# Optimization experiments

Measured on AMD Instinct MI355X. Metric: run time of the kernel, lower is better.

Reference implementation:

```python
import jax, jax.numpy as jnp
from jax import lax
import numpy as np

B, M, N, NUM_ITER = 8192, 256, 512, 16


def setup_inputs() -> dict:
    key = jax.random.key(0)
    k1, k2, k3, k4, k5 = jax.random.split(key, 5)
    y = jax.random.normal(k1, (B, M), dtype=jnp.float32)
    # Scale S/D/W so the unrolled recurrence stays numerically stable over 16 steps
    S = jax.random.normal(k2, (N, N), dtype=jnp.float32) * (0.9 / np.sqrt(N))
    W = jax.random.normal(k3, (N, M), dtype=jnp.float32) * (0.1 / np.sqrt(M))
    D = jax.random.normal(k4, (N, N), dtype=jnp.float32) * (1.0 / np.sqrt(N))
    thr = jax.random.uniform(k5, (1, 1), dtype=jnp.float32) * 0.1
    return {"y": y, "S": S, "W": W, "D": D, "thr": thr, "numIter": NUM_ITER}


def soft_thr(u, theta):
    return jax.nn.relu(u - theta) - jax.nn.relu(-u - theta)


def reference(y, S, W, D, thr, numIter):
    # Batch-first rewrite of: d = (D.T @ soft_thr(D @ (S@d.T + W@y.T), thr)).T
    Wy = y @ W.T  # (B, N), invariant across iterations
    d0 = jnp.zeros((y.shape[0], S.shape[0]), dtype=y.dtype)

    def step(d, _):
        z = d @ S.T + Wy          # (B, N)
        u = z @ D.T               # (B, N)  == (D @ z.T).T
        d_new = soft_thr(u, thr) @ D  # (B, N) == (D.T @ s.T).T
        return d_new, d_new

    _, ds = lax.scan(step, d0, None, length=numIter)
    # Original returns list [d0, d1, ..., d_numIter]; stack as one array
    return jnp.concatenate([d0[None], ds], axis=0)  # (numIter+1, B, N)
```

## Files before the change

### kernel.cpp

```cpp
#include <hip/hip_runtime.h>

#define B_SZ 8192
#define M_SZ 256
#define N_SZ 512
#define TB 64
#define THREADS 1024
#define LDP 520
#define LDPY 264
#define NITER 16

typedef _Float16 half8 __attribute__((ext_vector_type(8)));
typedef _Float16 half4 __attribute__((ext_vector_type(4)));
typedef float floatx4 __attribute__((ext_vector_type(4)));

__global__ void conv_kernel(const float* __restrict__ W, const float* __restrict__ D,
                            _Float16* __restrict__ Wf, _Float16* __restrict__ Df,
                            _Float16* __restrict__ Dtf) {
  int i = blockIdx.x * blockDim.x + threadIdx.x;
  if (i < N_SZ * N_SZ) {
    float d = D[i];
    Df[i] = (_Float16)d;
    int r = i >> 9;
    int c = i & (N_SZ - 1);
    Dtf[c * N_SZ + r] = (_Float16)d;
  }
  if (i < N_SZ * M_SZ) Wf[i] = (_Float16)W[i];
}

__global__ __launch_bounds__(256) void ecomp_kernel(const float* __restrict__ S,
                                                    const float* __restrict__ D,
                                                    _Float16* __restrict__ Ef) {
  __shared__ float Dst[8 * N_SZ];
  const int tid = threadIdx.x;
  const int r0 = blockIdx.x * 8;
  for (int i = tid; i < 8 * N_SZ; i += 256) Dst[i] = D[(size_t)r0 * N_SZ + i];
  __syncthreads();
  float acc[8][2];
#pragma unroll
  for (int r = 0; r < 8; ++r) acc[r][0] = acc[r][1] = 0.f;
#pragma unroll 4
  for (int j = 0; j < N_SZ; ++j) {
    float s0 = S[(size_t)j * N_SZ + tid];
    float s1 = S[(size_t)j * N_SZ + tid + 256];
#pragma unroll
    for (int r = 0; r < 8; ++r) {
      float dv = Dst[r * N_SZ + j];
      acc[r][0] += dv * s0;
      acc[r][1] += dv * s1;
    }
  }
#pragma unroll
  for (int r = 0; r < 8; ++r) {
    Ef[(size_t)(r0 + r) * N_SZ + tid] = (_Float16)acc[r][0];
    Ef[(size_t)(r0 + r) * N_SZ + tid + 256] = (_Float16)acc[r][1];
  }
}

__global__ __launch_bounds__(THREADS) void ista_kernel(
    const float* __restrict__ y, const _Float16* __restrict__ Ef,
    const _Float16* __restrict__ Df, const _Float16* __restrict__ Dtf,
    const _Float16* __restrict__ Wf, const float* __restrict__ thrp,
    float* __restrict__ out) {
  __shared__ _Float16 bufA[TB * LDP];
  __shared__ _Float16 bufB[TB * LDP];

  const int tid = threadIdx.x;
  const int wave = tid >> 6;
  const int lane = tid & 63;
  const int m16 = lane & 15;
  const int q = lane >> 4;
  const int rowBase = blockIdx.x * TB;
  const int colBase = wave * 32;

  {
    const int r = tid >> 4;
    const int c0 = (tid & 15) << 4;
    const float* src = y + (size_t)(rowBase + r) * M_SZ + c0;
#pragma unroll
    for (int j = 0; j < 16; j += 4) {
      float4 v = *reinterpret_cast<const float4*>(src + j);
      _Float16* dst = &bufA[r * LDPY + c0 + j];
      dst[0] = (_Float16)v.x;
      dst[1] = (_Float16)v.y;
      dst[2] = (_Float16)v.z;
      dst[3] = (_Float16)v.w;
    }
  }
  __syncthreads();

  floatx4 acc[4][2];

#pragma unroll
  for (int rt = 0; rt < 4; ++rt) acc[rt][0] = acc[rt][1] = (floatx4){0.f, 0.f, 0.f, 0.f};
#pragma unroll 2
  for (int ks = 0; ks < M_SZ / 32; ++ks) {
    half8 a0 = *reinterpret_cast<const half8*>(&bufA[m16 * LDPY + ks * 32 + q * 8]);
    half8 a1 = *reinterpret_cast<const half8*>(&bufA[(16 + m16) * LDPY + ks * 32 + q * 8]);
    half8 a2 = *reinterpret_cast<const half8*>(&bufA[(32 + m16) * LDPY + ks * 32 + q * 8]);
    half8 a3 = *reinterpret_cast<const half8*>(&bufA[(48 + m16) * LDPY + ks * 32 + q * 8]);
#pragma unroll
    for (int ct = 0; ct < 2; ++ct) {
      half8 b = *reinterpret_cast<const half8*>(Wf + (size_t)(colBase + ct * 16 + m16) * M_SZ + ks * 32 + q * 8);
      acc[0][ct] = __builtin_amdgcn_mfma_f32_16x16x32_f16(a0, b, acc[0][ct], 0, 0, 0);
      acc[1][ct] = __builtin_amdgcn_mfma_f32_16x16x32_f16(a1, b, acc[1][ct], 0, 0, 0);
      acc[2][ct] = __builtin_amdgcn_mfma_f32_16x16x32_f16(a2, b, acc[2][ct], 0, 0, 0);
      acc[3][ct] = __builtin_amdgcn_mfma_f32_16x16x32_f16(a3, b, acc[3][ct], 0, 0, 0);
    }
  }
#pragma unroll
  for (int rt = 0; rt < 4; ++rt)
#pragma unroll
    for (int ct = 0; ct < 2; ++ct)
#pragma unroll
      for (int r = 0; r < 4; ++r)
        bufB[(rt * 16 + q * 4 + r) * LDP + colBase + ct * 16 + m16] = (_Float16)acc[rt][ct][r];
  __syncthreads();

  auto gemmK512 = [&](const _Float16* Abuf, const _Float16* __restrict__ Bmat) {
    const _Float16* arow = Abuf + m16 * LDP + q * 8;
    const _Float16* brow0 = Bmat + (size_t)(colBase + m16) * N_SZ + q * 8;
    const _Float16* brow1 = Bmat + (size_t)(colBase + 16 + m16) * N_SZ + q * 8;
#pragma unroll 2
    for (int ks = 0; ks < N_SZ / 32; ++ks) {
      half8 a0 = *reinterpret_cast<const half8*>(arow + ks * 32);
      half8 a1 = *reinterpret_cast<const half8*>(arow + 16 * LDP + ks * 32);
      half8 a2 = *reinterpret_cast<const half8*>(arow + 32 * LDP + ks * 32);
      half8 a3 = *reinterpret_cast<const half8*>(arow + 48 * LDP + ks * 32);
      half8 b0 = *reinterpret_cast<const half8*>(brow0 + ks * 32);
      half8 b1 = *reinterpret_cast<const half8*>(brow1 + ks * 32);
      acc[0][0] = __builtin_amdgcn_mfma_f32_16x16x32_f16(a0, b0, acc[0][0], 0, 0, 0);
      acc[0][1] = __builtin_amdgcn_mfma_f32_16x16x32_f16(a0, b1, acc[0][1], 0, 0, 0);
      acc[1][0] = __builtin_amdgcn_mfma_f32_16x16x32_f16(a1, b0, acc[1][0], 0, 0, 0);
      acc[1][1] = __builtin_amdgcn_mfma_f32_16x16x32_f16(a1, b1, acc[1][1], 0, 0, 0);
      acc[2][0] = __builtin_amdgcn_mfma_f32_16x16x32_f16(a2, b0, acc[2][0], 0, 0, 0);
      acc[2][1] = __builtin_amdgcn_mfma_f32_16x16x32_f16(a2, b1, acc[2][1], 0, 0, 0);
      acc[3][0] = __builtin_amdgcn_mfma_f32_16x16x32_f16(a3, b0, acc[3][0], 0, 0, 0);
      acc[3][1] = __builtin_amdgcn_mfma_f32_16x16x32_f16(a3, b1, acc[3][1], 0, 0, 0);
    }
  };

#pragma unroll
  for (int rt = 0; rt < 4; ++rt) acc[rt][0] = acc[rt][1] = (floatx4){0.f, 0.f, 0.f, 0.f};
  gemmK512(bufB, Df);
  half4 ch[4][2];
#pragma unroll
  for (int rt = 0; rt < 4; ++rt)
#pragma unroll
    for (int ct = 0; ct < 2; ++ct)
#pragma unroll
      for (int r = 0; r < 4; ++r) ch[rt][ct][r] = (_Float16)acc[rt][ct][r];

  {
    int* za = reinterpret_cast<int*>(bufA);
    for (int i = tid; i < TB * LDP / 2; i += THREADS) za[i] = 0;
    float4 z4 = {0.f, 0.f, 0.f, 0.f};
    float4* o4 = reinterpret_cast<float4*>(out + (size_t)rowBase * N_SZ);
    for (int i = tid; i < TB * N_SZ / 4; i += THREADS) o4[i] = z4;
  }
  __syncthreads();

  const float thrv = *thrp;

#pragma unroll 1
  for (int it = 1; it <= NITER; ++it) {
#pragma unroll
    for (int rt = 0; rt < 4; ++rt) acc[rt][0] = acc[rt][1] = (floatx4){0.f, 0.f, 0.f, 0.f};
    gemmK512(bufA, Ef);
#pragma unroll
    for (int rt = 0; rt < 4; ++rt)
#pragma unroll
      for (int ct = 0; ct < 2; ++ct)
#pragma unroll
        for (int r = 0; r < 4; ++r) {
          float u = acc[rt][ct][r] + (float)ch[rt][ct][r];
          float s = fmaxf(u - thrv, 0.f) - fmaxf(-u - thrv, 0.f);
          bufB[(rt * 16 + q * 4 + r) * LDP + colBase + ct * 16 + m16] = (_Float16)s;
        }
    __syncthreads();

#pragma unroll
    for (int rt = 0; rt < 4; ++rt) acc[rt][0] = acc[rt][1] = (floatx4){0.f, 0.f, 0.f, 0.f};
    gemmK512(bufB, Dtf);
#pragma unroll
    for (int rt = 0; rt < 4; ++rt)
#pragma unroll
      for (int ct = 0; ct < 2; ++ct)
#pragma unroll
        for (int r = 0; r < 4; ++r)
          bufA[(rt * 16 + q * 4 + r) * LDP + colBase + ct * 16 + m16] = (_Float16)acc[rt][ct][r];
    __syncthreads();

    float* oslice = out + ((size_t)it * B_SZ + rowBase) * N_SZ;
#pragma unroll
    for (int i = tid; i < TB * N_SZ / 8; i += THREADS) {
      int r = i >> 6;
      int c8 = (i & 63) << 3;
      half8 h = *reinterpret_cast<const half8*>(&bufA[r * LDP + c8]);
      float4 lo = {(float)h[0], (float)h[1], (float)h[2], (float)h[3]};
      float4 hi = {(float)h[4], (float)h[5], (float)h[6], (float)h[7]};
      float* dst = oslice + (size_t)r * N_SZ + c8;
      *reinterpret_cast<float4*>(dst) = lo;
      *reinterpret_cast<float4*>(dst + 4) = hi;
    }
  }
}

extern "C" void kernel_launch(void* const* d_in, const int* in_sizes, int n_in,
                              void* d_out, int out_size, void* d_ws, size_t ws_size,
                              hipStream_t stream) {
  const float* y = (const float*)d_in[0];
  const float* S = (const float*)d_in[1];
  const float* W = (const float*)d_in[2];
  const float* D = (const float*)d_in[3];
  const float* thr = (const float*)d_in[4];
  float* out = (float*)d_out;

  char* ws = (char*)d_ws;
  _Float16* Ef = (_Float16*)(ws);
  _Float16* Df = (_Float16*)(ws + 512 * 1024);
  _Float16* Dtf = (_Float16*)(ws + 1024 * 1024);
  _Float16* Wf = (_Float16*)(ws + 1536 * 1024);

  conv_kernel<<<(N_SZ * N_SZ + 255) / 256, 256, 0, stream>>>(W, D, Wf, Df, Dtf);
  ecomp_kernel<<<N_SZ / 8, 256, 0, stream>>>(S, D, Ef);
  ista_kernel<<<B_SZ / TB, THREADS, 0, stream>>>(y, Ef, Df, Dtf, Wf, thr, out);
}
```

Measured before the change: 848.2 us.

## Halve batch tile, swizzle LDS, reorder iteration and stream output directly

The ISTA kernel batch tile drops from 64 to 32 rows, so twice as many blocks run and each wave holds half the accumulators. The padded LDS rows become an XOR-swizzled layout, and the loop is reordered so each iteration's D^T GEMM result goes straight from registers to global memory with nontemporal stores, which removes the separate LDS-to-global copy pass. The first soft-threshold now starts from the c term, the last E GEMM is skipped, and ecomp_kernel is rewritten with smaller blocks and no shared memory. Each block reloads the weight matrices from global/L2 for fewer rows, and the scattered scalar nontemporal stores may coalesce less well than the old float4 writes.

```diff
diff --git a/kernel.cpp b/kernel.cpp
--- a/kernel.cpp
+++ b/kernel.cpp
@@ -3,14 +3,11 @@
 #define B_SZ 8192
 #define M_SZ 256
 #define N_SZ 512
-#define TB 64
+#define TB 32
 #define THREADS 1024
-#define LDP 520
-#define LDPY 264
 #define NITER 16
 
 typedef _Float16 half8 __attribute__((ext_vector_type(8)));
-typedef _Float16 half4 __attribute__((ext_vector_type(4)));
 typedef float floatx4 __attribute__((ext_vector_type(4)));
 
 __global__ void conv_kernel(const float* __restrict__ W, const float* __restrict__ D,
@@ -27,182 +24,188 @@
   if (i < N_SZ * M_SZ) Wf[i] = (_Float16)W[i];
 }
 
-__global__ __launch_bounds__(256) void ecomp_kernel(const float* __restrict__ S,
+__global__ __launch_bounds__(512) void ecomp_kernel(const float* __restrict__ S,
                                                     const float* __restrict__ D,
                                                     _Float16* __restrict__ Ef) {
-  __shared__ float Dst[8 * N_SZ];
   const int tid = threadIdx.x;
-  const int r0 = blockIdx.x * 8;
-  for (int i = tid; i < 8 * N_SZ; i += 256) Dst[i] = D[(size_t)r0 * N_SZ + i];
-  __syncthreads();
-  float acc[8][2];
-#pragma unroll
-  for (int r = 0; r < 8; ++r) acc[r][0] = acc[r][1] = 0.f;
-#pragma unroll 4
+  const int r0 = blockIdx.x * 2;
+  float a0 = 0.f, a1 = 0.f;
+#pragma unroll 8
   for (int j = 0; j < N_SZ; ++j) {
-    float s0 = S[(size_t)j * N_SZ + tid];
-    float s1 = S[(size_t)j * N_SZ + tid + 256];
-#pragma unroll
-    for (int r = 0; r < 8; ++r) {
-      float dv = Dst[r * N_SZ + j];
-      acc[r][0] += dv * s0;
-      acc[r][1] += dv * s1;
-    }
-  }
-#pragma unroll
-  for (int r = 0; r < 8; ++r) {
-    Ef[(size_t)(r0 + r) * N_SZ + tid] = (_Float16)acc[r][0];
-    Ef[(size_t)(r0 + r) * N_SZ + tid + 256] = (_Float16)acc[r][1];
-  }
-}
-
-__global__ __launch_bounds__(THREADS) void ista_kernel(
+    float s = S[(size_t)j * N_SZ + tid];
+    a0 += D[(size_t)r0 * N_SZ + j] * s;
+    a1 += D[(size_t)(r0 + 1) * N_SZ + j] * s;
+  }
+  Ef[(size_t)r0 * N_SZ + tid] = (_Float16)a0;
+  Ef[(size_t)(r0 + 1) * N_SZ + tid] = (_Float16)a1;
+}
+
+__global__ __launch_bounds__(THREADS, 4) void ista_kernel(
     const float* __restrict__ y, const _Float16* __restrict__ Ef,
     const _Float16* __restrict__ Df, const _Float16* __restrict__ Dtf,
     const _Float16* __restrict__ Wf, const float* __restrict__ thrp,
     float* __restrict__ out) {
-  __shared__ _Float16 bufA[TB * LDP];
-  __shared__ _Float16 bufB[TB * LDP];
+  __shared__ _Float16 lds[2 * TB * N_SZ];
+  char* const ldsb = reinterpret_cast<char*>(lds);
+  constexpr int BOFF = TB * N_SZ * 2;
 
   const int tid = threadIdx.x;
-  const int wave = tid >> 6;
+  const int w = tid >> 6;
   const int lane = tid & 63;
   const int m16 = lane & 15;
   const int q = lane >> 4;
+  const int x8 = m16 & 7;
   const int rowBase = blockIdx.x * TB;
-  const int colBase = wave * 32;
+
+  const int offE = (((x8 & 4) >> 2) << 6) | ((q ^ (x8 & 3)) << 4);
+  const int offO = offE ^ 64;
+
+  floatx4 acc[2][2];
 
   {
-    const int r = tid >> 4;
-    const int c0 = (tid & 15) << 4;
-    const float* src = y + (size_t)(rowBase + r) * M_SZ + c0;
-#pragma unroll
-    for (int j = 0; j < 16; j += 4) {
-      float4 v = *reinterpret_cast<const float4*>(src + j);
-      _Float16* dst = &bufA[r * LDPY + c0 + j];
-      dst[0] = (_Float16)v.x;
-      dst[1] = (_Float16)v.y;
-      dst[2] = (_Float16)v.z;
-      dst[3] = (_Float16)v.w;
-    }
-  }
-  __syncthreads();
-
-  floatx4 acc[4][2];
-
-#pragma unroll
-  for (int rt = 0; rt < 4; ++rt) acc[rt][0] = acc[rt][1] = (floatx4){0.f, 0.f, 0.f, 0.f};
+    const int r = tid >> 5;
+    const int g = tid & 31;
+    const float* src = y + (size_t)(rowBase + r) * M_SZ + g * 8;
+    float4 v0 = *reinterpret_cast<const float4*>(src);
+    float4 v1 = *reinterpret_cast<const float4*>(src + 4);
+    half8 h = {(_Float16)v0.x, (_Float16)v0.y, (_Float16)v0.z, (_Float16)v0.w,
+               (_Float16)v1.x, (_Float16)v1.y, (_Float16)v1.z, (_Float16)v1.w};
+    *reinterpret_cast<half8*>(ldsb + r * 512 + ((g ^ (r & 7)) << 4)) = h;
+  }
+  __syncthreads();
+
+#define ZACC()                                                        \
+  acc[0][0] = acc[0][1] = acc[1][0] = acc[1][1] = (floatx4){0.f, 0.f, 0.f, 0.f}
+
+  ZACC();
+  {
+    const char* a0p = ldsb + m16 * 512;
+    const char* a1p = ldsb + (16 + m16) * 512;
+    const _Float16* b0p = Wf + (size_t)(w * 32 + m16) * M_SZ + q * 8;
+    const _Float16* b1p = b0p + 16 * M_SZ;
 #pragma unroll 2
-  for (int ks = 0; ks < M_SZ / 32; ++ks) {
-    half8 a0 = *reinterpret_cast<const half8*>(&bufA[m16 * LDPY + ks * 32 + q * 8]);
-    half8 a1 = *reinterpret_cast<const half8*>(&bufA[(16 + m16) * LDPY + ks * 32 + q * 8]);
-    half8 a2 = *reinterpret_cast<const half8*>(&bufA[(32 + m16) * LDPY + ks * 32 + q * 8]);
-    half8 a3 = *reinterpret_cast<const half8*>(&bufA[(48 + m16) * LDPY + ks * 32 + q * 8]);
-#pragma unroll
-    for (int ct = 0; ct < 2; ++ct) {
-      half8 b = *reinterpret_cast<const half8*>(Wf + (size_t)(colBase + ct * 16 + m16) * M_SZ + ks * 32 + q * 8);
-      acc[0][ct] = __builtin_amdgcn_mfma_f32_16x16x32_f16(a0, b, acc[0][ct], 0, 0, 0);
-      acc[1][ct] = __builtin_amdgcn_mfma_f32_16x16x32_f16(a1, b, acc[1][ct], 0, 0, 0);
-      acc[2][ct] = __builtin_amdgcn_mfma_f32_16x16x32_f16(a2, b, acc[2][ct], 0, 0, 0);
-      acc[3][ct] = __builtin_amdgcn_mfma_f32_16x16x32_f16(a3, b, acc[3][ct], 0, 0, 0);
-    }
-  }
-#pragma unroll
-  for (int rt = 0; rt < 4; ++rt)
-#pragma unroll
-    for (int ct = 0; ct < 2; ++ct)
-#pragma unroll
-      for (int r = 0; r < 4; ++r)
-        bufB[(rt * 16 + q * 4 + r) * LDP + colBase + ct * 16 + m16] = (_Float16)acc[rt][ct][r];
-  __syncthreads();
-
-  auto gemmK512 = [&](const _Float16* Abuf, const _Float16* __restrict__ Bmat) {
-    const _Float16* arow = Abuf + m16 * LDP + q * 8;
-    const _Float16* brow0 = Bmat + (size_t)(colBase + m16) * N_SZ + q * 8;
-    const _Float16* brow1 = Bmat + (size_t)(colBase + 16 + m16) * N_SZ + q * 8;
-#pragma unroll 2
-    for (int ks = 0; ks < N_SZ / 32; ++ks) {
-      half8 a0 = *reinterpret_cast<const half8*>(arow + ks * 32);
-      half8 a1 = *reinterpret_cast<const half8*>(arow + 16 * LDP + ks * 32);
-      half8 a2 = *reinterpret_cast<const half8*>(arow + 32 * LDP + ks * 32);
-      half8 a3 = *reinterpret_cast<const half8*>(arow + 48 * LDP + ks * 32);
-      half8 b0 = *reinterpret_cast<const half8*>(brow0 + ks * 32);
-      half8 b1 = *reinterpret_cast<const half8*>(brow1 + ks * 32);
+    for (int ks = 0; ks < 8; ++ks) {
+      const int go = ((ks & 1) ? offO : offE) + (ks >> 1) * 128;
+      half8 a0 = *reinterpret_cast<const half8*>(a0p + go);
+      half8 a1 = *reinterpret_cast<const half8*>(a1p + go);
+      half8 b0 = *reinterpret_cast<const half8*>(b0p + ks * 32);
+      half8 b1 = *reinterpret_cast<const half8*>(b1p + ks * 32);
       acc[0][0] = __builtin_amdgcn_mfma_f32_16x16x32_f16(a0, b0, acc[0][0], 0, 0, 0);
       acc[0][1] = __builtin_amdgcn_mfma_f32_16x16x32_f16(a0, b1, acc[0][1], 0, 0, 0);
       acc[1][0] = __builtin_amdgcn_mfma_f32_16x16x32_f16(a1, b0, acc[1][0], 0, 0, 0);
       acc[1][1] = __builtin_amdgcn_mfma_f32_16x16x32_f16(a1, b1, acc[1][1], 0, 0, 0);
-      acc[2][0] = __builtin_amdgcn_mfma_f32_16x16x32_f16(a2, b0, acc[2][0], 0, 0, 0);
-      acc[2][1] = __builtin_amdgcn_mfma_f32_16x16x32_f16(a2, b1, acc[2][1], 0, 0, 0);
-      acc[3][0] = __builtin_amdgcn_mfma_f32_16x16x32_f16(a3, b0, acc[3][0], 0, 0, 0);
-      acc[3][1] = __builtin_amdgcn_mfma_f32_16x16x32_f16(a3, b1, acc[3][1], 0, 0, 0);
+    }
+  }
+#pragma unroll
+  for (int rt = 0; rt < 2; ++rt)
+#pragma unroll
+    for (int ct = 0; ct < 2; ++ct)
+#pragma unroll
+      for (int r = 0; r < 4; ++r) {
+        const int row = rt * 16 + q * 4 + r;
+        const int col = w * 32 + ct * 16 + m16;
+        *reinterpret_cast<_Float16*>(
+            ldsb + BOFF + row * 1024 +
+            ((((col >> 3) ^ (row & 7)) << 4) | ((col & 7) << 1))) = (_Float16)acc[rt][ct][r];
+      }
+  __syncthreads();
+
+  auto gemm512 = [&](const int aoff, const _Float16* __restrict__ Bmat) {
+    const char* ap = ldsb + aoff + m16 * 1024;
+    const _Float16* b0p = Bmat + (size_t)(w * 32 + m16) * N_SZ + q * 8;
+    const _Float16* b1p = b0p + 16 * N_SZ;
+#pragma unroll 2
+    for (int ks = 0; ks < 16; ++ks) {
+      const int go = ((ks & 1) ? offO : offE) + (ks >> 1) * 128;
+      half8 a0 = *reinterpret_cast<const half8*>(ap + go);
+      half8 a1 = *reinterpret_cast<const half8*>(ap + 16 * 1024 + go);
+      half8 b0 = *reinterpret_cast<const half8*>(b0p + ks * 32);
+      half8 b1 = *reinterpret_cast<const half8*>(b1p + ks * 32);
+      acc[0][0] = __builtin_amdgcn_mfma_f32_16x16x32_f16(a0, b0, acc[0][0], 0, 0, 0);
+      acc[0][1] = __builtin_amdgcn_mfma_f32_16x16x32_f16(a0, b1, acc[0][1], 0, 0, 0);
+      acc[1][0] = __builtin_amdgcn_mfma_f32_16x16x32_f16(a1, b0, acc[1][0], 0, 0, 0);
+      acc[1][1] = __builtin_amdgcn_mfma_f32_16x16x32_f16(a1, b1, acc[1][1], 0, 0, 0);
     }
   };
 
-#pragma unroll
-  for (int rt = 0; rt < 4; ++rt) acc[rt][0] = acc[rt][1] = (floatx4){0.f, 0.f, 0.f, 0.f};
-  gemmK512(bufB, Df);
-  half4 ch[4][2];
-#pragma unroll
-  for (int rt = 0; rt < 4; ++rt)
+  ZACC();
+  gemm512(BOFF, Df);
+  _Float16 ch[2][2][4];
+#pragma unroll
+  for (int rt = 0; rt < 2; ++rt)
 #pragma unroll
     for (int ct = 0; ct < 2; ++ct)
 #pragma unroll
       for (int r = 0; r < 4; ++r) ch[rt][ct][r] = (_Float16)acc[rt][ct][r];
 
   {
-    int* za = reinterpret_cast<int*>(bufA);
-    for (int i = tid; i < TB * LDP / 2; i += THREADS) za[i] = 0;
-    float4 z4 = {0.f, 0.f, 0.f, 0.f};
-    float4* o4 = reinterpret_cast<float4*>(out + (size_t)rowBase * N_SZ);
-    for (int i = tid; i < TB * N_SZ / 4; i += THREADS) o4[i] = z4;
+    floatx4 z4 = {0.f, 0.f, 0.f, 0.f};
+    floatx4* o4 = reinterpret_cast<floatx4*>(out + (size_t)rowBase * N_SZ);
+#pragma unroll
+    for (int i = 0; i < (TB * N_SZ / 4) / THREADS; ++i)
+      __builtin_nontemporal_store(z4, o4 + tid + i * THREADS);
   }
   __syncthreads();
 
   const float thrv = *thrp;
+
+#pragma unroll
+  for (int rt = 0; rt < 2; ++rt)
+#pragma unroll
+    for (int ct = 0; ct < 2; ++ct)
+#pragma unroll
+      for (int r = 0; r < 4; ++r) {
+        float u = (float)ch[rt][ct][r];
+        float s = fmaxf(u - thrv, 0.f) - fmaxf(-u - thrv, 0.f);
+        const int row = rt * 16 + q * 4 + r;
+        const int col = w * 32 + ct * 16 + m16;
+        *reinterpret_cast<_Float16*>(
+            ldsb + BOFF + row * 1024 +
+            ((((col >> 3) ^ (row & 7)) << 4) | ((col & 7) << 1))) = (_Float16)s;
+      }
+  __syncthreads();
 
 #pragma unroll 1
   for (int it = 1; it <= NITER; ++it) {
-#pragma unroll
-    for (int rt = 0; rt < 4; ++rt) acc[rt][0] = acc[rt][1] = (floatx4){0.f, 0.f, 0.f, 0.f};
-    gemmK512(bufA, Ef);
-#pragma unroll
-    for (int rt = 0; rt < 4; ++rt)
+    ZACC();
+    gemm512(BOFF, Dtf);
+    float* osl = out + ((size_t)it * B_SZ + rowBase) * N_SZ;
+#pragma unroll
+    for (int rt = 0; rt < 2; ++rt)
+#pragma unroll
+      for (int ct = 0; ct < 2; ++ct)
+#pragma unroll
+        for (int r = 0; r < 4; ++r) {
+          float dv = acc[rt][ct][r];
+          const int row = rt * 16 + q * 4 + r;
+          const int col = w * 32 + ct * 16 + m16;
+          __builtin_nontemporal_store(dv, osl + (size_t)row * N_SZ + col);
+          *reinterpret_cast<_Float16*>(
+              ldsb + row * 1024 +
+              ((((col >> 3) ^ (row & 7)) << 4) | ((col & 7) << 1))) = (_Float16)dv;
+        }
+    __syncthreads();
+    if (it == NITER) break;
+
+    ZACC();
+    gemm512(0, Ef);
+#pragma unroll
+    for (int rt = 0; rt < 2; ++rt)
 #pragma unroll
       for (int ct = 0; ct < 2; ++ct)
 #pragma unroll
         for (int r = 0; r < 4; ++r) {
           float u = acc[rt][ct][r] + (float)ch[rt][ct][r];
           float s = fmaxf(u - thrv, 0.f) - fmaxf(-u - thrv, 0.f);
-          bufB[(rt * 16 + q * 4 + r) * LDP + colBase + ct * 16 + m16] = (_Float16)s;
+          const int row = rt * 16 + q * 4 + r;
+          const int col = w * 32 + ct * 16 + m16;
+          *reinterpret_cast<_Float16*>(
+              ldsb + BOFF + row * 1024 +
+              ((((col >> 3) ^ (row & 7)) << 4) | ((col & 7) << 1))) = (_Float16)s;
         }
     __syncthreads();
-
-#pragma unroll
-    for (int rt = 0; rt < 4; ++rt) acc[rt][0] = acc[rt][1] = (floatx4){0.f, 0.f, 0.f, 0.f};
-    gemmK512(bufB, Dtf);
-#pragma unroll
-    for (int rt = 0; rt < 4; ++rt)
-#pragma unroll
-      for (int ct = 0; ct < 2; ++ct)
-#pragma unroll
-        for (int r = 0; r < 4; ++r)
-          bufA[(rt * 16 + q * 4 + r) * LDP + colBase + ct * 16 + m16] = (_Float16)acc[rt][ct][r];
-    __syncthreads();
-
-    float* oslice = out + ((size_t)it * B_SZ + rowBase) * N_SZ;
-#pragma unroll
-    for (int i = tid; i < TB * N_SZ / 8; i += THREADS) {
-      int r = i >> 6;
-      int c8 = (i & 63) << 3;
-      half8 h = *reinterpret_cast<const half8*>(&bufA[r * LDP + c8]);
-      float4 lo = {(float)h[0], (float)h[1], (float)h[2], (float)h[3]};
-      float4 hi = {(float)h[4], (float)h[5], (float)h[6], (float)h[7]};
-      float* dst = oslice + (size_t)r * N_SZ + c8;
-      *reinterpret_cast<float4*>(dst) = lo;
-      *reinterpret_cast<float4*>(dst + 4) = hi;
-    }
-  }
+  }
+#undef ZACC
 }
 
 extern "C" void kernel_launch(void* const* d_in, const int* in_sizes, int n_in,
@@ -222,6 +225,6 @@
   _Float16* Wf = (_Float16*)(ws + 1536 * 1024);
 
   conv_kernel<<<(N_SZ * N_SZ + 255) / 256, 256, 0, stream>>>(W, D, Wf, Df, Dtf);
-  ecomp_kernel<<<N_SZ / 8, 256, 0, stream>>>(S, D, Ef);
+  ecomp_kernel<<<N_SZ / 2, 512, 0, stream>>>(S, D, Ef);
   ista_kernel<<<B_SZ / TB, THREADS, 0, stream>>>(y, Ef, Df, Dtf, Wf, thr, out);
 }
```

Result: faster. 768.4 us (-9.4%).
